# Performance work log

Measured on AMD Instinct MI355X. Metric: run time of the kernel, lower is better.

## Reference

```python
import jax, jax.numpy as jnp
import numpy as np

B, K, D = 131072, 1024, 128  # batch, codebook size, code dim


def setup_inputs() -> dict:
    key = jax.random.key(0)
    k1, k2 = jax.random.split(key)
    z_e = jax.random.normal(k1, (B, D), dtype=jnp.float32)
    # nn.Embedding weight init: uniform(-1/K, 1/K) as in TactileVQ.__init__
    codebook = jax.random.uniform(k2, (K, D), dtype=jnp.float32,
                                  minval=-1.0 / K, maxval=1.0 / K)
    return {"z_e": z_e, "codebook": codebook}


def reference(z_e, codebook):
    """TactileVQ forward: cdist(p=2) -> argmin -> codebook gather -> commitment MSE.
    Squared distances share the same argmin as euclidean cdist, so we use the
    expansion ||z||^2 - 2 z.E^T + ||E||^2 and never take a sqrt.
    """
    z_sq = jnp.sum(z_e * z_e, axis=-1, keepdims=True)          # [B, 1]
    e_sq = jnp.sum(codebook * codebook, axis=-1)               # [K]
    # [B, K] squared distances (monotone transform of cdist p=2)
    d2 = z_sq - 2.0 * jnp.einsum('bd,kd->bk', z_e, codebook) + e_sq
    encoding_indices = jnp.argmin(d2, axis=-1)                 # [B] int
    z_q = codebook[encoding_indices]                           # [B, D] gather
    commitment_loss = jnp.mean(
        (z_q - jax.lax.stop_gradient(z_e)) ** 2)               # mse vs detached z_e
    return z_q, commitment_loss, encoding_indices
```

## Files before the change

### kernel.cpp

```cpp
#include <hip/hip_runtime.h>
#include <math.h>

#define BN 131072
#define KN 1024
#define DN 128
#define GCODES 64
#define NGRP (KN / GCODES)

#define FROWS 256
#define FBLK (BN / FROWS)

#define ROWS 64
#define NBLK (BN / ROWS)

#define TAMB 2.5e-4f
#define CANARY 0.01f

typedef __attribute__((ext_vector_type(8))) short s16x8;
typedef __attribute__((ext_vector_type(4))) short s16x4;
typedef __attribute__((ext_vector_type(4))) float f32x4;

__device__ __forceinline__ unsigned short f2bf(float f) {
    const unsigned int u = __float_as_uint(f);
    return (unsigned short)((u + 0x7fffu + ((u >> 16) & 1u)) >> 16);
}
__device__ __forceinline__ float bf2f(unsigned short s) {
    return __uint_as_float(((unsigned int)s) << 16);
}
__device__ __forceinline__ void cvt4(const float4 v, s16x4& h4, s16x4& l4) {
    const unsigned short h0 = f2bf(v.x), h1 = f2bf(v.y), h2 = f2bf(v.z), h3 = f2bf(v.w);
    h4[0] = (short)h0; h4[1] = (short)h1; h4[2] = (short)h2; h4[3] = (short)h3;
    l4[0] = (short)f2bf(v.x - bf2f(h0));
    l4[1] = (short)f2bf(v.y - bf2f(h1));
    l4[2] = (short)f2bf(v.z - bf2f(h2));
    l4[3] = (short)f2bf(v.w - bf2f(h3));
}
__device__ __forceinline__ void cvt8(const float4 v0, const float4 v1,
                                     s16x8& h, s16x8& l) {
    s16x4 h0, l0, h1, l1;
    cvt4(v0, h0, l0); cvt4(v1, h1, l1);
    h[0]=h0[0]; h[1]=h0[1]; h[2]=h0[2]; h[3]=h0[3];
    h[4]=h1[0]; h[5]=h1[1]; h[6]=h1[2]; h[7]=h1[3];
    l[0]=l0[0]; l[1]=l0[1]; l[2]=l0[2]; l[3]=l0[3];
// ... 60 lines not shown
            a8[1] = __fadd_rn(a8[1], __fmul_rn(v0.y, v0.y));
            a8[2] = __fadd_rn(a8[2], __fmul_rn(v0.z, v0.z));
            a8[3] = __fadd_rn(a8[3], __fmul_rn(v0.w, v0.w));
            a8[4] = __fadd_rn(a8[4], __fmul_rn(v1.x, v1.x));
            a8[5] = __fadd_rn(a8[5], __fmul_rn(v1.y, v1.y));
            a8[6] = __fadd_rn(a8[6], __fmul_rn(v1.z, v1.z));
            a8[7] = __fadd_rn(a8[7], __fmul_rn(v1.w, v1.w));
        }
    }
    zsq[row] = __fadd_rn(
        __fadd_rn(__fadd_rn(a8[0], a8[1]), __fadd_rn(a8[2], a8[3])),
        __fadd_rn(__fadd_rn(a8[4], a8[5]), __fadd_rn(a8[6], a8[7])));
}

__device__ __forceinline__ float exact_d2_g(const float* __restrict__ z,
                                            const float* __restrict__ cb,
                                            const int grow, const int k,
                                            const float zsq, const float ek) {
    const float* zr = z + (size_t)grow * DN;
    const float* cr = cb + (size_t)k * DN;
    float dot = 0.0f;
#pragma unroll
    for (int j = 0; j < 32; ++j) {
        const float4 zv = *reinterpret_cast<const float4*>(zr + j * 4);
        const float4 cv = *reinterpret_cast<const float4*>(cr + j * 4);
        dot = __fmaf_rn(zv.x, cv.x, dot);
        dot = __fmaf_rn(zv.y, cv.y, dot);
        dot = __fmaf_rn(zv.z, cv.z, dot);
        dot = __fmaf_rn(zv.w, cv.w, dot);
    }
    return __fadd_rn(__fsub_rn(zsq, __fmul_rn(2.0f, dot)), ek);
}

__device__ __forceinline__ void tile_compute(const s16x8 (&ch)[4][4],
                                             const s16x8 (&cl)[4][4],
                                             const s16x8 (&zh)[4],
                                             const s16x8 (&zl)[4],
                                             const float (&ekv)[16],
                                             const int kbase, const int r0,
                                             float4* __restrict__ pq,
                                             const int l15, const int l4h) {
    f32x4 acc[4];
#pragma unroll
    for (int ct = 0; ct < 4; ++ct) acc[ct] = (f32x4){0.0f, 0.0f, 0.0f, 0.0f};
#pragma unroll
    for (int ks = 0; ks < 4; ++ks) {
#pragma unroll
        for (int ct = 0; ct < 4; ++ct) {
            acc[ct] = __builtin_amdgcn_mfma_f32_16x16x32_bf16(ch[ct][ks], zh[ks], acc[ct], 0, 0, 0);
            acc[ct] = __builtin_amdgcn_mfma_f32_16x16x32_bf16(cl[ct][ks], zh[ks], acc[ct], 0, 0, 0);
            acc[ct] = __builtin_amdgcn_mfma_f32_16x16x32_bf16(ch[ct][ks], zl[ks], acc[ct], 0, 0, 0);
        }
    }
    float b1 = INFINITY, b2 = INFINITY, b3 = INFINITY;
    int   i1 = 0, i2 = 0;
#pragma unroll
    for (int ct = 0; ct < 4; ++ct) {
#pragma unroll
        for (int e = 0; e < 4; ++e) {
            const float sc = __fmaf_rn(-2.0f, acc[ct][e], ekv[ct * 4 + e]);
            const int   kk = kbase + ct * 16 + l4h * 4 + e;
            const bool lt1 = sc < b1;
            const bool lt2 = sc < b2;
            const bool lt3 = sc < b3;
            b3 = lt2 ? b2 : (lt3 ? sc : b3);
            b2 = lt1 ? b1 : (lt2 ? sc : b2);
            i2 = lt1 ? i1 : (lt2 ? kk : i2);
            b1 = lt1 ? sc : b1;
            i1 = lt1 ? kk : i1;
        }
    }
#pragma unroll
    for (int st = 16; st < 64; st <<= 1) {
        const float ob1 = __shfl_xor(b1, st);
        const int   oi1 = __shfl_xor(i1, st);
        const float ob2 = __shfl_xor(b2, st);
        const int   oi2 = __shfl_xor(i2, st);
        const float ob3 = __shfl_xor(b3, st);
        float v1, v2, v3; int j1, j2;
        if (ob1 < b1) {
            v1 = ob1; j1 = oi1;
            if (b1 < ob2) { v2 = b1;  j2 = i1;  v3 = fminf(b2, ob2); }
            else          { v2 = ob2; j2 = oi2; v3 = fminf(b1, ob3); }
        } else {
            v1 = b1; j1 = i1;
            if (ob1 < b2) { v2 = ob1; j2 = oi1; v3 = fminf(ob2, b2); }
            else          { v2 = b2;  j2 = i2;  v3 = fminf(ob1, b3); }
        }
        b1 = v1; i1 = j1; b2 = v2; i2 = j2; b3 = v3;
    }
    if (l4h == 0) {
        float4 q;
        q.x = b1; q.y = b2; q.z = b3;
        q.w = __int_as_float((i2 << 16) | i1);
        pq[r0 + l15] = q;
    }
}

__device__ __forceinline__ void tile_load_zp(const unsigned short* __restrict__ zb,
                                             s16x8 (&zh)[4], s16x8 (&zl)[4]) {
#pragma unroll
    for (int ks = 0; ks < 4; ++ks) {
        zh[ks] = *reinterpret_cast<const s16x8*>(zb + ks * 512);
        zl[ks] = *reinterpret_cast<const s16x8*>(zb + 2048 + ks * 512);
    }
}

__global__ __launch_bounds__(256, 2) void vq_score_pre(const unsigned short* __restrict__ zp,
                                                       const unsigned short* __restrict__ planes,
                                                       const float* __restrict__ esq,
                                                       float4* __restrict__ pquad) {
    const int tid  = threadIdx.x;
    const int lane = tid & 63;
    const int w    = tid >> 6;
    const int l15  = lane & 15;
    const int l4h  = lane >> 4;
    const int sliceW = blockIdx.x >> 7;
    const int chunk  = blockIdx.x & 127;
    const int sub    = sliceW * 4 + w;
    const int kbase  = sub * 64;

    s16x8 ch[4][4], cl[4][4];
    {
        const unsigned short* gp = planes + (size_t)sub * 16384;
#pragma unroll
        for (int ks = 0; ks < 4; ++ks)
#pragma unroll
            for (int ct = 0; ct < 4; ++ct) {
                const int off = ((((ks * 4 + l4h) << 6) + (ct << 4) + l15) << 3);
                ch[ct][ks] = *reinterpret_cast<const s16x8*>(gp + off);
                cl[ct][ks] = *reinterpret_cast<const s16x8*>(gp + 8192 + off);
            }
    }
    float ekv[16];
#pragma unroll
    for (int ct = 0; ct < 4; ++ct)
#pragma unroll
        for (int e = 0; e < 4; ++e)
            ekv[ct * 4 + e] = esq[kbase + ct * 16 + l4h * 4 + e];

    const int cbase = chunk * 64;
    const int rbase = chunk * 1024;
    float4* pq = pquad + (size_t)sub * BN;
    const unsigned short* zpl = zp + l4h * 128 + l15 * 8;

    s16x8 hA[4], lA[4], hB[4], lB[4];
    tile_load_zp(zpl + (size_t)cbase * 4096, hA, lA);
#pragma unroll 1
    for (int t = 0; t < 64; t += 2) {
        tile_load_zp(zpl + (size_t)(cbase + t + 1) * 4096, hB, lB);
        tile_compute(ch, cl, hA, lA, ekv, kbase, rbase + t * 16, pq, l15, l4h);
        const int tn = (t + 2 < 64) ? t + 2 : 63;
        tile_load_zp(zpl + (size_t)(cbase + tn) * 4096, hA, lA);
        tile_compute(ch, cl, hB, lB, ekv, kbase, rbase + (t + 1) * 16, pq, l15, l4h);
    }
}

__global__ __launch_bounds__(256, 2) void vq_score(const float* __restrict__ z,
                                                   const unsigned short* __restrict__ planes,
                                                   const float* __restrict__ esq,
                                                   float4* __restrict__ pquad) {
    const int tid  = threadIdx.x;
    const int lane = tid & 63;
    const int w    = tid >> 6;
    const int l15  = lane & 15;
    const int l4h  = lane >> 4;
    const int sliceW = blockIdx.x >> 7;
    const int chunk  = blockIdx.x & 127;
    const int sub    = sliceW * 4 + w;
    const int kbase  = sub * 64;

    s16x8 ch[4][4], cl[4][4];
    {
        const unsigned short* gp = planes + (size_t)sub * 16384;
#pragma unroll
        for (int ks = 0; ks < 4; ++ks)
#pragma unroll
            for (int ct = 0; ct < 4; ++ct) {
                const int off = ((((ks * 4 + l4h) << 6) + (ct << 4) + l15) << 3);
                ch[ct][ks] = *reinterpret_cast<const s16x8*>(gp + off);
                cl[ct][ks] = *reinterpret_cast<const s16x8*>(gp + 8192 + off);
            }
    }
    float ekv[16];
#pragma unroll
    for (int ct = 0; ct < 4; ++ct)
#pragma unroll
        for (int e = 0; e < 4; ++e)
            ekv[ct * 4 + e] = esq[kbase + ct * 16 + l4h * 4 + e];

    const int rbase = chunk * 1024;
    float4* pq = pquad + (size_t)sub * BN;

#pragma unroll 1
    for (int t = 0; t < 64; ++t) {
        const int r0 = rbase + t * 16;
        s16x8 zh[4], zl[4];
#pragma unroll
        for (int ks = 0; ks < 4; ++ks) {
            const float* src = z + (size_t)(r0 + l15) * DN + ks * 32 + l4h * 8;
            const float4 v0 = *reinterpret_cast<const float4*>(src);
            const float4 v1 = *reinterpret_cast<const float4*>(src + 4);
            cvt8(v0, v1, zh[ks], zl[ks]);
        }
        tile_compute(ch, cl, zh, zl, ekv, kbase, r0, pq, l15, l4h);
    }
}

template <bool HZ>
__global__ __launch_bounds__(256, 2) void vq_finish2(const float* __restrict__ z,
                                                     const float* __restrict__ cb,
                                                     const float* __restrict__ esq,
                                                     const float* __restrict__ zsqArr,
                                                     const float4* __restrict__ pquad,
                                                     float* __restrict__ out,
                                                     double* __restrict__ partials) {
    __shared__ __align__(16) float sEsq[KN];
    __shared__ float  szsq[FROWS];
    __shared__ int    sbidx[FROWS], sI1[FROWS], sI2[FROWS];
    __shared__ int    t2list[FROWS], t3list[FROWS];
    __shared__ int    t2n, t3n, sbad;
    __shared__ double sls[256];

    const int tid  = threadIdx.x;
    const int lane = tid & 63;
    const int w    = tid >> 6;
    const int row0 = blockIdx.x * FROWS;

    if (tid == 0) { t2n = 0; t3n = 0; sbad = 0; }
#pragma unroll
    for (int i = 0; i < 4; ++i) sEsq[i * 256 + tid] = esq[i * 256 + tid];

    if constexpr (HZ) {
        szsq[tid] = zsqArr[row0 + tid];
    } else {
        const float* zr = z + (size_t)(row0 + tid) * DN;
        float a8[8];
#pragma unroll
        for (int c = 0; c < 32; ++c) {
            const float4 v = *reinterpret_cast<const float4*>(zr + c * 4);
            const int t0 = 4 * (c & 1);
            if (c < 2) {
                a8[t0 + 0] = __fmul_rn(v.x, v.x);
                a8[t0 + 1] = __fmul_rn(v.y, v.y);
                a8[t0 + 2] = __fmul_rn(v.z, v.z);
                a8[t0 + 3] = __fmul_rn(v.w, v.w);
            } else {
                a8[t0 + 0] = __fadd_rn(a8[t0 + 0], __fmul_rn(v.x, v.x));
                a8[t0 + 1] = __fadd_rn(a8[t0 + 1], __fmul_rn(v.y, v.y));
                a8[t0 + 2] = __fadd_rn(a8[t0 + 2], __fmul_rn(v.z, v.z));
                a8[t0 + 3] = __fadd_rn(a8[t0 + 3], __fmul_rn(v.w, v.w));
            }
        }
        szsq[tid] = __fadd_rn(
            __fadd_rn(__fadd_rn(a8[0], a8[1]), __fadd_rn(a8[2], a8[3])),
            __fadd_rn(__fadd_rn(a8[4], a8[5]), __fadd_rn(a8[6], a8[7])));
    }
    __syncthreads();

    float B1 = INFINITY, B2 = INFINITY, B3 = INFINITY;
    int   I1 = 0, I2 = 0;
    {
        const int r = row0 + tid;
#pragma unroll
        for (int s = 0; s < 16; ++s) {
            const float4 q = pquad[(size_t)s * BN + r];
            const int ii = __float_as_int(q.w);
            const int j1 = ii & 0xffff, j2 = ii >> 16;
            if (q.x < B1)      { B3 = B2; B2 = B1; I2 = I1; B1 = q.x; I1 = j1; }
            else if (q.x < B2) { B3 = B2; B2 = q.x; I2 = j1; }
            else if (q.x < B3) { B3 = q.x; }
            if (q.y < B2)      { B3 = B2; B2 = q.y; I2 = j2; }
            else if (q.y < B3) { B3 = q.y; }
            B3 = fminf(B3, q.z);
        }
        sbidx[tid] = I1; sI1[tid] = I1; sI2[tid] = I2;
        if ((tid & 63) == 0) {
            const float d2x  = exact_d2_g(z, cb, r, I1, szsq[tid], sEsq[I1]);
            const float pred = __fadd_rn(szsq[tid], B1);
            if (fabsf(pred - d2x) > CANARY) sbad = 1;
        }
    }
    __syncthreads();

    if (sbad) {
        for (int r = w; r < FROWS; r += 4) {
            const float zsq = szsq[r];
            float best = INFINITY; int bi = 0;
#pragma unroll 1
            for (int kk = 0; kk < 16; ++kk) {
                const int k = lane * 16 + kk;
                const float d2v = exact_d2_g(z, cb, row0 + r, k, zsq, sEsq[k]);
                if (d2v < best) { best = d2v; bi = k; }
            }
#pragma unroll
            for (int m = 1; m < 64; m <<= 1) {
                const float ob  = __shfl_xor(best, m);
                const int   obi = __shfl_xor(bi, m);
                if (ob < best || (ob == best && obi < bi)) { best = ob; bi = obi; }
            }
            if (lane == 0) sbidx[r] = bi;
        }
    } else {
        if (B3 - B1 <= TAMB) {
            const int p = atomicAdd(&t3n, 1); t3list[p] = tid;
        } else if (B2 - B1 <= TAMB) {
            const int p = atomicAdd(&t2n, 1); t2list[p] = tid;
        }
    }
    __syncthreads();

    if (tid < t2n) {
        const int r  = t2list[tid];
        const int ka = sI1[r], kb = sI2[r];
        const float zsq = szsq[r];
        const float da = exact_d2_g(z, cb, row0 + r, ka, zsq, sEsq[ka]);
        const float db = exact_d2_g(z, cb, row0 + r, kb, zsq, sEsq[kb]);
        int win;
        if (da < db) win = ka;
        else if (db < da) win = kb;
        else win = (ka < kb) ? ka : kb;
        sbidx[r] = win;
    }
    for (int ii = w; ii < t3n; ii += 4) {
        const int r = t3list[ii];
        const float zsq = szsq[r];
        float best = INFINITY; int bi = 0;
#pragma unroll 1
        for (int kk = 0; kk < 16; ++kk) {
            const int k = lane * 16 + kk;
            const float d2v = exact_d2_g(z, cb, row0 + r, k, zsq, sEsq[k]);
            if (d2v < best) { best = d2v; bi = k; }
        }
#pragma unroll
        for (int m = 1; m < 64; m <<= 1) {
            const float ob  = __shfl_xor(best, m);
            const int   obi = __shfl_xor(bi, m);
            if (ob < best || (ob == best && obi < bi)) { best = ob; bi = obi; }
        }
        if (lane == 0) sbidx[r] = bi;
    }
    __syncthreads();

    out[(size_t)BN * DN + 1 + row0 + tid] = (float)sbidx[tid];

    double ls = 0.0;
#pragma unroll
    for (int it = 0; it < 32; ++it) {
        const int r = it * 8 + (tid >> 5);
        const int j = tid & 31;
        const float4 zv = *reinterpret_cast<const float4*>(
            z + ((size_t)(row0 + r)) * DN + j * 4);
        const int bfin = sbidx[r];
        const float4 cv = *reinterpret_cast<const float4*>(
            cb + ((size_t)bfin) * DN + j * 4);
        *reinterpret_cast<float4*>(out + ((size_t)(row0 + r)) * DN + j * 4) = cv;
        const float d0 = __fsub_rn(cv.x, zv.x);
        const float d1 = __fsub_rn(cv.y, zv.y);
        const float d2e = __fsub_rn(cv.z, zv.z);
        const float d3 = __fsub_rn(cv.w, zv.w);
        ls += (double)__fmul_rn(d0, d0);
        ls += (double)__fmul_rn(d1, d1);
        ls += (double)__fmul_rn(d2e, d2e);
        ls += (double)__fmul_rn(d3, d3);
    }
    sls[tid] = ls;
    __syncthreads();
    for (int s = 128; s > 0; s >>= 1) {
        if (tid < s) sls[tid] += sls[tid + s];
        __syncthreads();
    }
    if (tid == 0) partials[blockIdx.x] = sls[0];
}

#define UPD(s, sc, kk) { \
    const bool lt1 = (sc) < b1v[s]; \
    const bool lt2 = (sc) < b2v[s]; \
    const bool lt3 = (sc) < b3v[s]; \
    b3v[s] = lt2 ? b2v[s] : (lt3 ? (sc) : b3v[s]); \
    b2v[s] = lt1 ? b1v[s] : (lt2 ? (sc) : b2v[s]); \
    i2v[s] = lt1 ? i1v[s] : (lt2 ? (kk) : i2v[s]); \
    b1v[s] = lt1 ? (sc) : b1v[s]; \
    i1v[s] = lt1 ? (kk) : i1v[s]; }

__global__ __launch_bounds__(256, 2) void vq_lds(const float* __restrict__ z,
                                                 const float* __restrict__ cb,
                                                 const float* __restrict__ esq,
                                                 float* __restrict__ out,
                                                 double* __restrict__ partials) {
    __shared__ __align__(16) short cbS[2][16384];
    __shared__ __align__(16) float sEsq[KN];
    __shared__ float  szsq[ROWS];
    __shared__ float  sB1[2][ROWS], sB2[2][ROWS], sB3[2][ROWS];
    __shared__ int    sI1[2][ROWS], sI2[2][ROWS];
    __shared__ int    sbidx[ROWS];
    __shared__ int    t2list[ROWS], t3list[ROWS];
    __shared__ int    t2n, t3n;
// ... 285 lines not shown
__global__ __launch_bounds__(256) void loss_kernel(const double* __restrict__ partials,
                                                   float* __restrict__ out, int n) {
    __shared__ double s[256];
    double acc = 0.0;
    for (int i = threadIdx.x; i < n; i += 256) acc += partials[i];
    s[threadIdx.x] = acc;
    __syncthreads();
    for (int t = 128; t > 0; t >>= 1) {
        if (threadIdx.x < t) s[threadIdx.x] += s[threadIdx.x + t];
        __syncthreads();
    }
    if (threadIdx.x == 0)
        out[(size_t)BN * DN] = (float)(s[0] / ((double)BN * (double)DN));
}

extern "C" void kernel_launch(void* const* d_in, const int* in_sizes, int n_in,
                              void* d_out, int out_size, void* d_ws, size_t ws_size,
                              hipStream_t stream) {
    const float* z  = (const float*)d_in[0];
    const float* cb = (const float*)d_in[1];
    float* out = (float*)d_out;

    float*          esq      = (float*)d_ws;
    double*         partials = (double*)((char*)d_ws + 4096);
    unsigned short* cbpl     = (unsigned short*)((char*)d_ws + 20480);
    float4*         pquad    = (float4*)((char*)d_ws + 544768);
    float*          zsqArr   = (float*)((char*)d_ws + 34099200ull);
    unsigned short* zpl      = (unsigned short*)((char*)d_ws + 34623488ull);
    const size_t need_mid  = 34099200ull;
    const size_t need_full = 101732352ull;

    esq_kernel<<<KN / 256, 256, 0, stream>>>(cb, esq);
    if (ws_size >= need_full) {
        cvt_kernel <<<64, 256, 0, stream>>>(cb, cbpl);
        zprep_kernel<<<BN / 256, 256, 0, stream>>>(z, zpl, zsqArr);
        vq_score_pre<<<512, 256, 0, stream>>>(zpl, cbpl, esq, pquad);
        vq_finish2<true><<<FBLK, 256, 0, stream>>>(z, cb, esq, zsqArr, pquad, out, partials);
        loss_kernel<<<1, 256, 0, stream>>>(partials, out, FBLK);
    } else if (ws_size >= need_mid) {
        cvt_kernel<<<64, 256, 0, stream>>>(cb, cbpl);
        vq_score  <<<512, 256, 0, stream>>>(z, cbpl, esq, pquad);
        vq_finish2<false><<<FBLK, 256, 0, stream>>>(z, cb, esq, nullptr, pquad, out, partials);
        loss_kernel<<<1, 256, 0, stream>>>(partials, out, FBLK);
    } else {
        vq_lds<<<NBLK, 256, 0, stream>>>(z, cb, esq, out, partials);
        loss_kernel<<<1, 256, 0, stream>>>(partials, out, NBLK);
    }
}
```

Baseline: 261.0 us.

## Split finish-kernel candidate merge across two thread halves and raise MFMA priority

The finish kernel now handles 128 rows per block instead of 256. Each row's 16 partial top-3 candidate lists are split between two threads, each scanning 8 of them, and the halves are merged through shared memory. This doubles the number of blocks and raises the occupancy hint so more loads are in flight. It also moves tie classification before the first barrier, removing one sync, and wraps the MFMA block in s_setprio so matrix instructions get issue priority. The cost is the extra LDS traffic for the merge, with half the threads idle during scalar phases.

```diff
diff --git a/kernel.cpp b/kernel.cpp
--- a/kernel.cpp
+++ b/kernel.cpp
@@ -7,8 +7,8 @@
 #define GCODES 64
 #define NGRP (KN / GCODES)
 
-#define FROWS 256
-#define FBLK (BN / FROWS)
+#define F3ROWS 128
+#define F3BLK (BN / F3ROWS)
 
 #define ROWS 64
 #define NBLK (BN / ROWS)
@@ -146,6 +146,7 @@
     f32x4 acc[4];
 #pragma unroll
     for (int ct = 0; ct < 4; ++ct) acc[ct] = (f32x4){0.0f, 0.0f, 0.0f, 0.0f};
+    __builtin_amdgcn_s_setprio(1);
 #pragma unroll
     for (int ks = 0; ks < 4; ++ks) {
 #pragma unroll
@@ -155,6 +156,7 @@
             acc[ct] = __builtin_amdgcn_mfma_f32_16x16x32_bf16(ch[ct][ks], zl[ks], acc[ct], 0, 0, 0);
         }
     }
+    __builtin_amdgcn_s_setprio(0);
     float b1 = INFINITY, b2 = INFINITY, b3 = INFINITY;
     int   i1 = 0, i2 = 0;
 #pragma unroll
@@ -311,7 +313,7 @@
 }
 
 template <bool HZ>
-__global__ __launch_bounds__(256, 2) void vq_finish2(const float* __restrict__ z,
+__global__ __launch_bounds__(256, 4) void vq_finish3(const float* __restrict__ z,
                                                      const float* __restrict__ cb,
                                                      const float* __restrict__ esq,
                                                      const float* __restrict__ zsqArr,
@@ -319,75 +321,106 @@
                                                      float* __restrict__ out,
                                                      double* __restrict__ partials) {
     __shared__ __align__(16) float sEsq[KN];
-    __shared__ float  szsq[FROWS];
-    __shared__ int    sbidx[FROWS], sI1[FROWS], sI2[FROWS];
-    __shared__ int    t2list[FROWS], t3list[FROWS];
+    __shared__ float  szsq[F3ROWS];
+    __shared__ float  hB1[F3ROWS], hB2[F3ROWS], hB3[F3ROWS];
+    __shared__ int    hI1[F3ROWS], hI2[F3ROWS];
+    __shared__ int    sbidx[F3ROWS], sI1[F3ROWS], sI2[F3ROWS];
+    __shared__ int    t2list[F3ROWS], t3list[F3ROWS];
     __shared__ int    t2n, t3n, sbad;
     __shared__ double sls[256];
 
-    const int tid  = threadIdx.x;
-    const int lane = tid & 63;
-    const int w    = tid >> 6;
-    const int row0 = blockIdx.x * FROWS;
+    const int tid   = threadIdx.x;
+    const int lane  = tid & 63;
+    const int w     = tid >> 6;
+    const int rloc  = tid & 127;
+    const int shalf = tid >> 7;
+    const int row0  = blockIdx.x * F3ROWS;
 
     if (tid == 0) { t2n = 0; t3n = 0; sbad = 0; }
 #pragma unroll
     for (int i = 0; i < 4; ++i) sEsq[i * 256 + tid] = esq[i * 256 + tid];
 
-    if constexpr (HZ) {
-        szsq[tid] = zsqArr[row0 + tid];
-    } else {
-        const float* zr = z + (size_t)(row0 + tid) * DN;
-        float a8[8];
-#pragma unroll
-        for (int c = 0; c < 32; ++c) {
-            const float4 v = *reinterpret_cast<const float4*>(zr + c * 4);
-            const int t0 = 4 * (c & 1);
-            if (c < 2) {
-                a8[t0 + 0] = __fmul_rn(v.x, v.x);
-                a8[t0 + 1] = __fmul_rn(v.y, v.y);
-                a8[t0 + 2] = __fmul_rn(v.z, v.z);
-                a8[t0 + 3] = __fmul_rn(v.w, v.w);
-            } else {
-                a8[t0 + 0] = __fadd_rn(a8[t0 + 0], __fmul_rn(v.x, v.x));
-                a8[t0 + 1] = __fadd_rn(a8[t0 + 1], __fmul_rn(v.y, v.y));
-                a8[t0 + 2] = __fadd_rn(a8[t0 + 2], __fmul_rn(v.z, v.z));
-                a8[t0 + 3] = __fadd_rn(a8[t0 + 3], __fmul_rn(v.w, v.w));
-            }
-        }
-        szsq[tid] = __fadd_rn(
-            __fadd_rn(__fadd_rn(a8[0], a8[1]), __fadd_rn(a8[2], a8[3])),
-            __fadd_rn(__fadd_rn(a8[4], a8[5]), __fadd_rn(a8[6], a8[7])));
-    }
-    __syncthreads();
-
-    float B1 = INFINITY, B2 = INFINITY, B3 = INFINITY;
-    int   I1 = 0, I2 = 0;
+    if (tid < F3ROWS) {
+        if constexpr (HZ) {
+            szsq[tid] = zsqArr[row0 + tid];
+        } else {
+            const float* zr = z + (size_t)(row0 + tid) * DN;
+            float a8[8];
+#pragma unroll
+            for (int c = 0; c < 32; ++c) {
+                const float4 v = *reinterpret_cast<const float4*>(zr + c * 4);
+                const int t0 = 4 * (c & 1);
+                if (c < 2) {
+                    a8[t0 + 0] = __fmul_rn(v.x, v.x);
+                    a8[t0 + 1] = __fmul_rn(v.y, v.y);
+                    a8[t0 + 2] = __fmul_rn(v.z, v.z);
+                    a8[t0 + 3] = __fmul_rn(v.w, v.w);
+                } else {
+                    a8[t0 + 0] = __fadd_rn(a8[t0 + 0], __fmul_rn(v.x, v.x));
+                    a8[t0 + 1] = __fadd_rn(a8[t0 + 1], __fmul_rn(v.y, v.y));
+                    a8[t0 + 2] = __fadd_rn(a8[t0 + 2], __fmul_rn(v.z, v.z));
+                    a8[t0 + 3] = __fadd_rn(a8[t0 + 3], __fmul_rn(v.w, v.w));
+                }
+            }
+            szsq[tid] = __fadd_rn(
+                __fadd_rn(__fadd_rn(a8[0], a8[1]), __fadd_rn(a8[2], a8[3])),
+                __fadd_rn(__fadd_rn(a8[4], a8[5]), __fadd_rn(a8[6], a8[7])));
+        }
+    }
+
+    float b1 = INFINITY, b2 = INFINITY, b3 = INFINITY;
+    int   i1 = 0, i2 = 0;
     {
-        const int r = row0 + tid;
-#pragma unroll
-        for (int s = 0; s < 16; ++s) {
-            const float4 q = pquad[(size_t)s * BN + r];
+        const int r  = row0 + rloc;
+        const int s0 = shalf * 8;
+#pragma unroll
+        for (int s = 0; s < 8; ++s) {
+            const float4 q = pquad[(size_t)(s0 + s) * BN + r];
             const int ii = __float_as_int(q.w);
             const int j1 = ii & 0xffff, j2 = ii >> 16;
-            if (q.x < B1)      { B3 = B2; B2 = B1; I2 = I1; B1 = q.x; I1 = j1; }
-            else if (q.x < B2) { B3 = B2; B2 = q.x; I2 = j1; }
-            else if (q.x < B3) { B3 = q.x; }
-            if (q.y < B2)      { B3 = B2; B2 = q.y; I2 = j2; }
-            else if (q.y < B3) { B3 = q.y; }
-            B3 = fminf(B3, q.z);
+            if (q.x < b1)      { b3 = b2; b2 = b1; i2 = i1; b1 = q.x; i1 = j1; }
+            else if (q.x < b2) { b3 = b2; b2 = q.x; i2 = j1; }
+            else if (q.x < b3) { b3 = q.x; }
+            if (q.y < b2)      { b3 = b2; b2 = q.y; i2 = j2; }
+            else if (q.y < b3) { b3 = q.y; }
+            b3 = fminf(b3, q.z);
+        }
+    }
+    if (shalf) {
+        hB1[rloc] = b1; hB2[rloc] = b2; hB3[rloc] = b3;
+        hI1[rloc] = i1; hI2[rloc] = i2;
+    }
+    __syncthreads();
+
+    float B1, B2, B3; int I1, I2;
+    if (tid < F3ROWS) {
+        const float c1 = hB1[tid], c2 = hB2[tid], c3 = hB3[tid];
+        const int  cj1 = hI1[tid], cj2 = hI2[tid];
+        if (b1 <= c1) {
+            B1 = b1; I1 = i1;
+            if (b2 <= c1) { B2 = b2; I2 = i2;  B3 = fminf(b3, c1); }
+            else          { B2 = c1; I2 = cj1; B3 = fminf(b2, c2); }
+        } else {
+            B1 = c1; I1 = cj1;
+            if (c2 <= b1) { B2 = c2; I2 = cj2; B3 = fminf(c3, b1); }
+            else          { B2 = b1; I2 = i1;  B3 = fminf(c2, b2); }
         }
         sbidx[tid] = I1; sI1[tid] = I1; sI2[tid] = I2;
         if ((tid & 63) == 0) {
-            const float d2x  = exact_d2_g(z, cb, r, I1, szsq[tid], sEsq[I1]);
+            const float d2x  = exact_d2_g(z, cb, row0 + tid, I1, szsq[tid], sEsq[I1]);
             const float pred = __fadd_rn(szsq[tid], B1);
             if (fabsf(pred - d2x) > CANARY) sbad = 1;
         }
+        if (B3 - B1 <= TAMB) {
+            const int p = atomicAdd(&t3n, 1); t3list[p] = tid;
+        } else if (B2 - B1 <= TAMB) {
+            const int p = atomicAdd(&t2n, 1); t2list[p] = tid;
+        }
     }
     __syncthreads();
 
     if (sbad) {
-        for (int r = w; r < FROWS; r += 4) {
+        for (int r = w; r < F3ROWS; r += 4) {
             const float zsq = szsq[r];
             float best = INFINITY; int bi = 0;
 #pragma unroll 1
@@ -405,51 +438,45 @@
             if (lane == 0) sbidx[r] = bi;
         }
     } else {
-        if (B3 - B1 <= TAMB) {
-            const int p = atomicAdd(&t3n, 1); t3list[p] = tid;
-        } else if (B2 - B1 <= TAMB) {
-            const int p = atomicAdd(&t2n, 1); t2list[p] = tid;
-        }
-    }
-    __syncthreads();
-
-    if (tid < t2n) {
-        const int r  = t2list[tid];
-        const int ka = sI1[r], kb = sI2[r];
-        const float zsq = szsq[r];
-        const float da = exact_d2_g(z, cb, row0 + r, ka, zsq, sEsq[ka]);
-        const float db = exact_d2_g(z, cb, row0 + r, kb, zsq, sEsq[kb]);
-        int win;
-        if (da < db) win = ka;
-        else if (db < da) win = kb;
-        else win = (ka < kb) ? ka : kb;
-        sbidx[r] = win;
-    }
-    for (int ii = w; ii < t3n; ii += 4) {
-        const int r = t3list[ii];
-        const float zsq = szsq[r];
-        float best = INFINITY; int bi = 0;
+        if (tid < t2n) {
+            const int r  = t2list[tid];
+            const int ka = sI1[r], kb = sI2[r];
+            const float zsq = szsq[r];
+            const float da = exact_d2_g(z, cb, row0 + r, ka, zsq, sEsq[ka]);
+            const float db = exact_d2_g(z, cb, row0 + r, kb, zsq, sEsq[kb]);
+            int win;
+            if (da < db) win = ka;
+            else if (db < da) win = kb;
+            else win = (ka < kb) ? ka : kb;
+            sbidx[r] = win;
+        }
+        for (int ii = w; ii < t3n; ii += 4) {
+            const int r = t3list[ii];
+            const float zsq = szsq[r];
+            float best = INFINITY; int bi = 0;
 #pragma unroll 1
-        for (int kk = 0; kk < 16; ++kk) {
-            const int k = lane * 16 + kk;
-            const float d2v = exact_d2_g(z, cb, row0 + r, k, zsq, sEsq[k]);
-            if (d2v < best) { best = d2v; bi = k; }
-        }
-#pragma unroll
-        for (int m = 1; m < 64; m <<= 1) {
-            const float ob  = __shfl_xor(best, m);
-            const int   obi = __shfl_xor(bi, m);
-            if (ob < best || (ob == best && obi < bi)) { best = ob; bi = obi; }
-        }
-        if (lane == 0) sbidx[r] = bi;
-    }
-    __syncthreads();
-
-    out[(size_t)BN * DN + 1 + row0 + tid] = (float)sbidx[tid];
+            for (int kk = 0; kk < 16; ++kk) {
+                const int k = lane * 16 + kk;
+                const float d2v = exact_d2_g(z, cb, row0 + r, k, zsq, sEsq[k]);
+                if (d2v < best) { best = d2v; bi = k; }
+            }
+#pragma unroll
+            for (int m = 1; m < 64; m <<= 1) {
+                const float ob  = __shfl_xor(best, m);
+                const int   obi = __shfl_xor(bi, m);
+                if (ob < best || (ob == best && obi < bi)) { best = ob; bi = obi; }
+            }
+            if (lane == 0) sbidx[r] = bi;
+        }
+    }
+    __syncthreads();
+
+    if (tid < F3ROWS)
+        out[(size_t)BN * DN + 1 + row0 + tid] = (float)sbidx[tid];
 
     double ls = 0.0;
 #pragma unroll
-    for (int it = 0; it < 32; ++it) {
+    for (int it = 0; it < 16; ++it) {
         const int r = it * 8 + (tid >> 5);
         const int j = tid & 31;
         const float4 zv = *reinterpret_cast<const float4*>(
@@ -820,13 +847,13 @@
         cvt_kernel <<<64, 256, 0, stream>>>(cb, cbpl);
         zprep_kernel<<<BN / 256, 256, 0, stream>>>(z, zpl, zsqArr);
         vq_score_pre<<<512, 256, 0, stream>>>(zpl, cbpl, esq, pquad);
-        vq_finish2<true><<<FBLK, 256, 0, stream>>>(z, cb, esq, zsqArr, pquad, out, partials);
-        loss_kernel<<<1, 256, 0, stream>>>(partials, out, FBLK);
+        vq_finish3<true><<<F3BLK, 256, 0, stream>>>(z, cb, esq, zsqArr, pquad, out, partials);
+        loss_kernel<<<1, 256, 0, stream>>>(partials, out, F3BLK);
     } else if (ws_size >= need_mid) {
         cvt_kernel<<<64, 256, 0, stream>>>(cb, cbpl);
         vq_score  <<<512, 256, 0, stream>>>(z, cbpl, esq, pquad);
-        vq_finish2<false><<<FBLK, 256, 0, stream>>>(z, cb, esq, nullptr, pquad, out, partials);
-        loss_kernel<<<1, 256, 0, stream>>>(partials, out, FBLK);
+        vq_finish3<false><<<F3BLK, 256, 0, stream>>>(z, cb, esq, nullptr, pquad, out, partials);
+        loss_kernel<<<1, 256, 0, stream>>>(partials, out, F3BLK);
     } else {
         vq_lds<<<NBLK, 256, 0, stream>>>(z, cb, esq, out, partials);
         loss_kernel<<<1, 256, 0, stream>>>(partials, out, NBLK);
```

After: 279.2 us. 7.0% more time.

## Stage codebook slice in LDS, split finish into merge and epilogue kernels

Applied to the files above, without the earlier changes.

The scoring kernel now loads each 64-code bf16 hi/lo slice into shared memory instead of registers. It raises occupancy to 3 blocks per SM, processes two z tiles per iteration sharing the codebook fragment loads, and wraps the MFMA loop in s_setprio. The finish kernel is split into a merge kernel that writes indices and a separate epilogue that gathers codes, writes z_q and reduces the loss over smaller 64-row blocks. The merge also prefetches all 16 partial quads before reducing them. This trades register pressure for LDS reads and adds a launch plus a round trip of the indices through global memory.

```diff
diff --git a/kernel.cpp b/kernel.cpp
--- a/kernel.cpp
+++ b/kernel.cpp
@@ -7,8 +7,11 @@
 #define GCODES 64
 #define NGRP (KN / GCODES)
 
-#define FROWS 256
-#define FBLK (BN / FROWS)
+#define MROWS 256
+#define MBLK (BN / MROWS)
+
+#define EROWS 64
+#define EBLK (BN / EROWS)
 
 #define ROWS 64
 #define NBLK (BN / ROWS)
@@ -135,26 +138,11 @@
     return __fadd_rn(__fsub_rn(zsq, __fmul_rn(2.0f, dot)), ek);
 }
 
-__device__ __forceinline__ void tile_compute(const s16x8 (&ch)[4][4],
-                                             const s16x8 (&cl)[4][4],
-                                             const s16x8 (&zh)[4],
-                                             const s16x8 (&zl)[4],
-                                             const float (&ekv)[16],
-                                             const int kbase, const int r0,
-                                             float4* __restrict__ pq,
-                                             const int l15, const int l4h) {
-    f32x4 acc[4];
-#pragma unroll
-    for (int ct = 0; ct < 4; ++ct) acc[ct] = (f32x4){0.0f, 0.0f, 0.0f, 0.0f};
-#pragma unroll
-    for (int ks = 0; ks < 4; ++ks) {
-#pragma unroll
-        for (int ct = 0; ct < 4; ++ct) {
-            acc[ct] = __builtin_amdgcn_mfma_f32_16x16x32_bf16(ch[ct][ks], zh[ks], acc[ct], 0, 0, 0);
-            acc[ct] = __builtin_amdgcn_mfma_f32_16x16x32_bf16(cl[ct][ks], zh[ks], acc[ct], 0, 0, 0);
-            acc[ct] = __builtin_amdgcn_mfma_f32_16x16x32_bf16(ch[ct][ks], zl[ks], acc[ct], 0, 0, 0);
-        }
-    }
+__device__ __forceinline__ void fin_store(const f32x4 (&acc)[4],
+                                          const float (&ekv)[16],
+                                          const int kbase, const int r0,
+                                          float4* __restrict__ pq,
+                                          const int l15, const int l4h) {
     float b1 = INFINITY, b2 = INFINITY, b3 = INFINITY;
     int   i1 = 0, i2 = 0;
 #pragma unroll
@@ -200,62 +188,78 @@
     }
 }
 
-__device__ __forceinline__ void tile_load_zp(const unsigned short* __restrict__ zb,
-                                             s16x8 (&zh)[4], s16x8 (&zl)[4]) {
-#pragma unroll
-    for (int ks = 0; ks < 4; ++ks) {
-        zh[ks] = *reinterpret_cast<const s16x8*>(zb + ks * 512);
-        zl[ks] = *reinterpret_cast<const s16x8*>(zb + 2048 + ks * 512);
-    }
-}
-
-__global__ __launch_bounds__(256, 2) void vq_score_pre(const unsigned short* __restrict__ zp,
-                                                       const unsigned short* __restrict__ planes,
+__global__ __launch_bounds__(256, 3) void vq_score_lds(const unsigned short* __restrict__ zp,
+                                                       const unsigned short* __restrict__ cbpl,
                                                        const float* __restrict__ esq,
                                                        float4* __restrict__ pquad) {
+    __shared__ __align__(16) short cbS[16384];
     const int tid  = threadIdx.x;
     const int lane = tid & 63;
     const int w    = tid >> 6;
     const int l15  = lane & 15;
     const int l4h  = lane >> 4;
-    const int sliceW = blockIdx.x >> 7;
-    const int chunk  = blockIdx.x & 127;
-    const int sub    = sliceW * 4 + w;
-    const int kbase  = sub * 64;
-
-    s16x8 ch[4][4], cl[4][4];
+    const int sub   = blockIdx.x >> 7;
+    const int chunk = blockIdx.x & 127;
+    const int kbase = sub * 64;
+
     {
-        const unsigned short* gp = planes + (size_t)sub * 16384;
-#pragma unroll
-        for (int ks = 0; ks < 4; ++ks)
+        const float4* src = reinterpret_cast<const float4*>(cbpl + (size_t)sub * 16384);
+        float4* dst = reinterpret_cast<float4*>(cbS);
+#pragma unroll
+        for (int i = 0; i < 8; ++i)
+            dst[i * 256 + tid] = src[i * 256 + tid];
+    }
+    float ekv[16];
+#pragma unroll
+    for (int ct = 0; ct < 4; ++ct)
+#pragma unroll
+        for (int e = 0; e < 4; ++e)
+            ekv[ct * 4 + e] = esq[kbase + ct * 16 + l4h * 4 + e];
+    __syncthreads();
+
+    const int tbase = chunk * 64 + w * 16;
+    float4* pq = pquad + (size_t)sub * BN;
+    const unsigned short* zpl = zp + l4h * 128 + l15 * 8;
+
+#pragma unroll 1
+    for (int tp = 0; tp < 16; tp += 2) {
+        s16x8 zh[2][4], zl[2][4];
+#pragma unroll
+        for (int u = 0; u < 2; ++u) {
+            const unsigned short* zb = zpl + (size_t)(tbase + tp + u) * 4096;
+#pragma unroll
+            for (int ks = 0; ks < 4; ++ks) {
+                zh[u][ks] = *reinterpret_cast<const s16x8*>(zb + ks * 512);
+                zl[u][ks] = *reinterpret_cast<const s16x8*>(zb + 2048 + ks * 512);
+            }
+        }
+        f32x4 acc[2][4];
+#pragma unroll
+        for (int u = 0; u < 2; ++u)
+#pragma unroll
+            for (int ct = 0; ct < 4; ++ct)
+                acc[u][ct] = (f32x4){0.0f, 0.0f, 0.0f, 0.0f};
+
+        __builtin_amdgcn_s_setprio(1);
+#pragma unroll
+        for (int ks = 0; ks < 4; ++ks) {
 #pragma unroll
             for (int ct = 0; ct < 4; ++ct) {
                 const int off = ((((ks * 4 + l4h) << 6) + (ct << 4) + l15) << 3);
-                ch[ct][ks] = *reinterpret_cast<const s16x8*>(gp + off);
-                cl[ct][ks] = *reinterpret_cast<const s16x8*>(gp + 8192 + off);
-            }
-    }
-    float ekv[16];
-#pragma unroll
-    for (int ct = 0; ct < 4; ++ct)
-#pragma unroll
-        for (int e = 0; e < 4; ++e)
-            ekv[ct * 4 + e] = esq[kbase + ct * 16 + l4h * 4 + e];
-
-    const int cbase = chunk * 64;
-    const int rbase = chunk * 1024;
-    float4* pq = pquad + (size_t)sub * BN;
-    const unsigned short* zpl = zp + l4h * 128 + l15 * 8;
-
-    s16x8 hA[4], lA[4], hB[4], lB[4];
-    tile_load_zp(zpl + (size_t)cbase * 4096, hA, lA);
-#pragma unroll 1
-    for (int t = 0; t < 64; t += 2) {
-        tile_load_zp(zpl + (size_t)(cbase + t + 1) * 4096, hB, lB);
-        tile_compute(ch, cl, hA, lA, ekv, kbase, rbase + t * 16, pq, l15, l4h);
-        const int tn = (t + 2 < 64) ? t + 2 : 63;
-        tile_load_zp(zpl + (size_t)(cbase + tn) * 4096, hA, lA);
-        tile_compute(ch, cl, hB, lB, ekv, kbase, rbase + (t + 1) * 16, pq, l15, l4h);
+                const s16x8 bh = *reinterpret_cast<const s16x8*>(&cbS[off]);
+                const s16x8 bl = *reinterpret_cast<const s16x8*>(&cbS[8192 + off]);
+                acc[0][ct] = __builtin_amdgcn_mfma_f32_16x16x32_bf16(bh, zh[0][ks], acc[0][ct], 0, 0, 0);
+                acc[0][ct] = __builtin_amdgcn_mfma_f32_16x16x32_bf16(bl, zh[0][ks], acc[0][ct], 0, 0, 0);
+                acc[0][ct] = __builtin_amdgcn_mfma_f32_16x16x32_bf16(bh, zl[0][ks], acc[0][ct], 0, 0, 0);
+                acc[1][ct] = __builtin_amdgcn_mfma_f32_16x16x32_bf16(bh, zh[1][ks], acc[1][ct], 0, 0, 0);
+                acc[1][ct] = __builtin_amdgcn_mfma_f32_16x16x32_bf16(bl, zh[1][ks], acc[1][ct], 0, 0, 0);
+                acc[1][ct] = __builtin_amdgcn_mfma_f32_16x16x32_bf16(bh, zl[1][ks], acc[1][ct], 0, 0, 0);
+            }
+        }
+        __builtin_amdgcn_s_setprio(0);
+
+        fin_store(acc[0], ekv, kbase, (tbase + tp) * 16,     pq, l15, l4h);
+        fin_store(acc[1], ekv, kbase, (tbase + tp + 1) * 16, pq, l15, l4h);
     }
 }
 
@@ -306,29 +310,41 @@
             const float4 v1 = *reinterpret_cast<const float4*>(src + 4);
             cvt8(v0, v1, zh[ks], zl[ks]);
         }
-        tile_compute(ch, cl, zh, zl, ekv, kbase, r0, pq, l15, l4h);
+        f32x4 acc[4];
+#pragma unroll
+        for (int ct = 0; ct < 4; ++ct) acc[ct] = (f32x4){0.0f, 0.0f, 0.0f, 0.0f};
+        __builtin_amdgcn_s_setprio(1);
+#pragma unroll
+        for (int ks = 0; ks < 4; ++ks) {
+#pragma unroll
+            for (int ct = 0; ct < 4; ++ct) {
+                acc[ct] = __builtin_amdgcn_mfma_f32_16x16x32_bf16(ch[ct][ks], zh[ks], acc[ct], 0, 0, 0);
+                acc[ct] = __builtin_amdgcn_mfma_f32_16x16x32_bf16(cl[ct][ks], zh[ks], acc[ct], 0, 0, 0);
+                acc[ct] = __builtin_amdgcn_mfma_f32_16x16x32_bf16(ch[ct][ks], zl[ks], acc[ct], 0, 0, 0);
+            }
+        }
+        __builtin_amdgcn_s_setprio(0);
+        fin_store(acc, ekv, kbase, r0, pq, l15, l4h);
     }
 }
 
 template <bool HZ>
-__global__ __launch_bounds__(256, 2) void vq_finish2(const float* __restrict__ z,
-                                                     const float* __restrict__ cb,
-                                                     const float* __restrict__ esq,
-                                                     const float* __restrict__ zsqArr,
-                                                     const float4* __restrict__ pquad,
-                                                     float* __restrict__ out,
-                                                     double* __restrict__ partials) {
+__global__ __launch_bounds__(256, 2) void vq_merge(const float* __restrict__ z,
+                                                   const float* __restrict__ cb,
+                                                   const float* __restrict__ esq,
+                                                   const float* __restrict__ zsqArr,
+                                                   const float4* __restrict__ pquad,
+                                                   float* __restrict__ out) {
     __shared__ __align__(16) float sEsq[KN];
-    __shared__ float  szsq[FROWS];
-    __shared__ int    sbidx[FROWS], sI1[FROWS], sI2[FROWS];
-    __shared__ int    t2list[FROWS], t3list[FROWS];
+    __shared__ float  szsq[MROWS];
+    __shared__ int    sbidx[MROWS], sI1[MROWS], sI2[MROWS];
+    __shared__ int    t2list[MROWS], t3list[MROWS];
     __shared__ int    t2n, t3n, sbad;
-    __shared__ double sls[256];
 
     const int tid  = threadIdx.x;
     const int lane = tid & 63;
     const int w    = tid >> 6;
-    const int row0 = blockIdx.x * FROWS;
+    const int row0 = blockIdx.x * MROWS;
 
     if (tid == 0) { t2n = 0; t3n = 0; sbad = 0; }
 #pragma unroll
@@ -365,17 +381,20 @@
     int   I1 = 0, I2 = 0;
     {
         const int r = row0 + tid;
+        float4 q[16];
+#pragma unroll
+        for (int s = 0; s < 16; ++s)
+            q[s] = pquad[(size_t)s * BN + r];
 #pragma unroll
         for (int s = 0; s < 16; ++s) {
-            const float4 q = pquad[(size_t)s * BN + r];
-            const int ii = __float_as_int(q.w);
+            const int ii = __float_as_int(q[s].w);
             const int j1 = ii & 0xffff, j2 = ii >> 16;
-            if (q.x < B1)      { B3 = B2; B2 = B1; I2 = I1; B1 = q.x; I1 = j1; }
-            else if (q.x < B2) { B3 = B2; B2 = q.x; I2 = j1; }
-            else if (q.x < B3) { B3 = q.x; }
-            if (q.y < B2)      { B3 = B2; B2 = q.y; I2 = j2; }
-            else if (q.y < B3) { B3 = q.y; }
-            B3 = fminf(B3, q.z);
+            if (q[s].x < B1)      { B3 = B2; B2 = B1; I2 = I1; B1 = q[s].x; I1 = j1; }
+            else if (q[s].x < B2) { B3 = B2; B2 = q[s].x; I2 = j1; }
+            else if (q[s].x < B3) { B3 = q[s].x; }
+            if (q[s].y < B2)      { B3 = B2; B2 = q[s].y; I2 = j2; }
+            else if (q[s].y < B3) { B3 = q[s].y; }
+            B3 = fminf(B3, q[s].z);
         }
         sbidx[tid] = I1; sI1[tid] = I1; sI2[tid] = I2;
         if ((tid & 63) == 0) {
@@ -387,7 +406,7 @@
     __syncthreads();
 
     if (sbad) {
-        for (int r = w; r < FROWS; r += 4) {
+        for (int r = w; r < MROWS; r += 4) {
             const float zsq = szsq[r];
             float best = INFINITY; int bi = 0;
 #pragma unroll 1
@@ -446,26 +465,48 @@
     __syncthreads();
 
     out[(size_t)BN * DN + 1 + row0 + tid] = (float)sbidx[tid];
+}
+
+__global__ __launch_bounds__(256, 4) void vq_epilogue(const float* __restrict__ z,
+                                                      const float* __restrict__ cb,
+                                                      float* __restrict__ out,
+                                                      double* __restrict__ partials) {
+    __shared__ int sidx[EROWS];
+    __shared__ double sls[256];
+    const int tid  = threadIdx.x;
+    const int row0 = blockIdx.x * EROWS;
+
+    if (tid < EROWS)
+        sidx[tid] = (int)out[(size_t)BN * DN + 1 + row0 + tid];
+    __syncthreads();
 
     double ls = 0.0;
-#pragma unroll
-    for (int it = 0; it < 32; ++it) {
-        const int r = it * 8 + (tid >> 5);
-        const int j = tid & 31;
-        const float4 zv = *reinterpret_cast<const float4*>(
-            z + ((size_t)(row0 + r)) * DN + j * 4);
-        const int bfin = sbidx[r];
-        const float4 cv = *reinterpret_cast<const float4*>(
-            cb + ((size_t)bfin) * DN + j * 4);
-        *reinterpret_cast<float4*>(out + ((size_t)(row0 + r)) * DN + j * 4) = cv;
-        const float d0 = __fsub_rn(cv.x, zv.x);
-        const float d1 = __fsub_rn(cv.y, zv.y);
-        const float d2e = __fsub_rn(cv.z, zv.z);
-        const float d3 = __fsub_rn(cv.w, zv.w);
-        ls += (double)__fmul_rn(d0, d0);
-        ls += (double)__fmul_rn(d1, d1);
-        ls += (double)__fmul_rn(d2e, d2e);
-        ls += (double)__fmul_rn(d3, d3);
+    const int j = tid & 31;
+#pragma unroll
+    for (int half = 0; half < 2; ++half) {
+        float4 zb[4], cv[4];
+        int rr[4];
+#pragma unroll
+        for (int u = 0; u < 4; ++u) {
+            const int it = half * 4 + u;
+            rr[u] = it * 8 + (tid >> 5);
+            zb[u] = *reinterpret_cast<const float4*>(
+                z + (size_t)(row0 + rr[u]) * DN + j * 4);
+            cv[u] = *reinterpret_cast<const float4*>(
+                cb + (size_t)sidx[rr[u]] * DN + j * 4);
+        }
+#pragma unroll
+        for (int u = 0; u < 4; ++u) {
+            *reinterpret_cast<float4*>(out + (size_t)(row0 + rr[u]) * DN + j * 4) = cv[u];
+            const float d0 = __fsub_rn(cv[u].x, zb[u].x);
+            const float d1 = __fsub_rn(cv[u].y, zb[u].y);
+            const float d2e = __fsub_rn(cv[u].z, zb[u].z);
+            const float d3 = __fsub_rn(cv[u].w, zb[u].w);
+            ls += (double)__fmul_rn(d0, d0);
+            ls += (double)__fmul_rn(d1, d1);
+            ls += (double)__fmul_rn(d2e, d2e);
+            ls += (double)__fmul_rn(d3, d3);
+        }
     }
     sls[tid] = ls;
     __syncthreads();
@@ -817,16 +858,18 @@
 
     esq_kernel<<<KN / 256, 256, 0, stream>>>(cb, esq);
     if (ws_size >= need_full) {
-        cvt_kernel <<<64, 256, 0, stream>>>(cb, cbpl);
+        cvt_kernel  <<<64, 256, 0, stream>>>(cb, cbpl);
         zprep_kernel<<<BN / 256, 256, 0, stream>>>(z, zpl, zsqArr);
-        vq_score_pre<<<512, 256, 0, stream>>>(zpl, cbpl, esq, pquad);
-        vq_finish2<true><<<FBLK, 256, 0, stream>>>(z, cb, esq, zsqArr, pquad, out, partials);
-        loss_kernel<<<1, 256, 0, stream>>>(partials, out, FBLK);
+        vq_score_lds<<<2048, 256, 0, stream>>>(zpl, cbpl, esq, pquad);
+        vq_merge<true><<<MBLK, 256, 0, stream>>>(z, cb, esq, zsqArr, pquad, out);
+        vq_epilogue <<<EBLK, 256, 0, stream>>>(z, cb, out, partials);
+        loss_kernel <<<1, 256, 0, stream>>>(partials, out, EBLK);
     } else if (ws_size >= need_mid) {
         cvt_kernel<<<64, 256, 0, stream>>>(cb, cbpl);
         vq_score  <<<512, 256, 0, stream>>>(z, cbpl, esq, pquad);
-        vq_finish2<false><<<FBLK, 256, 0, stream>>>(z, cb, esq, nullptr, pquad, out, partials);
-        loss_kernel<<<1, 256, 0, stream>>>(partials, out, FBLK);
+        vq_merge<false><<<MBLK, 256, 0, stream>>>(z, cb, esq, nullptr, pquad, out);
+        vq_epilogue<<<EBLK, 256, 0, stream>>>(z, cb, out, partials);
+        loss_kernel<<<1, 256, 0, stream>>>(partials, out, EBLK);
     } else {
         vq_lds<<<NBLK, 256, 0, stream>>>(z, cb, esq, out, partials);
         loss_kernel<<<1, 256, 0, stream>>>(partials, out, NBLK);
```

After: 555.5 us. +112.8%, slower.

## Split finish kernel into merge and epilogue kernels with smaller blocks

Applied to the files above, without the earlier changes.

Splits the combined finish kernel into two launches. vq_merge uses 128-row blocks to merge the partial top-k scores and refine ambiguous rows; it reads esq straight from global memory instead of staging it in LDS, and batches its pquad loads. vq_epilogue uses 64-row blocks to do the codebook gather, the output write and the loss partials, reading the indices back from the output buffer. The aim is more blocks and better latency hiding in the memory-bound tail, at the cost of an extra launch and re-reading the indices.

```diff
diff --git a/kernel.cpp b/kernel.cpp
--- a/kernel.cpp
+++ b/kernel.cpp
@@ -7,8 +7,11 @@
 #define GCODES 64
 #define NGRP (KN / GCODES)
 
-#define FROWS 256
-#define FBLK (BN / FROWS)
+#define MROWS 128
+#define MBLK (BN / MROWS)
+
+#define EROWS 64
+#define EBLK (BN / EROWS)
 
 #define ROWS 64
 #define NBLK (BN / ROWS)
@@ -311,33 +314,29 @@
 }
 
 template <bool HZ>
-__global__ __launch_bounds__(256, 2) void vq_finish2(const float* __restrict__ z,
-                                                     const float* __restrict__ cb,
-                                                     const float* __restrict__ esq,
-                                                     const float* __restrict__ zsqArr,
-                                                     const float4* __restrict__ pquad,
-                                                     float* __restrict__ out,
-                                                     double* __restrict__ partials) {
-    __shared__ __align__(16) float sEsq[KN];
-    __shared__ float  szsq[FROWS];
-    __shared__ int    sbidx[FROWS], sI1[FROWS], sI2[FROWS];
-    __shared__ int    t2list[FROWS], t3list[FROWS];
+__global__ __launch_bounds__(128, 4) void vq_merge(const float* __restrict__ z,
+                                                   const float* __restrict__ cb,
+                                                   const float* __restrict__ esq,
+                                                   const float* __restrict__ zsqArr,
+                                                   const float4* __restrict__ pquad,
+                                                   float* __restrict__ out) {
+    __shared__ float  szsq[MROWS];
+    __shared__ int    sbidx[MROWS], sI1[MROWS], sI2[MROWS];
+    __shared__ int    t2list[MROWS], t3list[MROWS];
     __shared__ int    t2n, t3n, sbad;
-    __shared__ double sls[256];
 
     const int tid  = threadIdx.x;
     const int lane = tid & 63;
     const int w    = tid >> 6;
-    const int row0 = blockIdx.x * FROWS;
+    const int row0 = blockIdx.x * MROWS;
+    const int r    = row0 + tid;
 
     if (tid == 0) { t2n = 0; t3n = 0; sbad = 0; }
-#pragma unroll
-    for (int i = 0; i < 4; ++i) sEsq[i * 256 + tid] = esq[i * 256 + tid];
 
     if constexpr (HZ) {
-        szsq[tid] = zsqArr[row0 + tid];
+        szsq[tid] = zsqArr[r];
     } else {
-        const float* zr = z + (size_t)(row0 + tid) * DN;
+        const float* zr = z + (size_t)r * DN;
         float a8[8];
 #pragma unroll
         for (int c = 0; c < 32; ++c) {
@@ -363,37 +362,40 @@
 
     float B1 = INFINITY, B2 = INFINITY, B3 = INFINITY;
     int   I1 = 0, I2 = 0;
-    {
-        const int r = row0 + tid;
-#pragma unroll
-        for (int s = 0; s < 16; ++s) {
-            const float4 q = pquad[(size_t)s * BN + r];
-            const int ii = __float_as_int(q.w);
+#pragma unroll
+    for (int half = 0; half < 2; ++half) {
+        float4 q[8];
+#pragma unroll
+        for (int s = 0; s < 8; ++s)
+            q[s] = pquad[(size_t)(half * 8 + s) * BN + r];
+#pragma unroll
+        for (int s = 0; s < 8; ++s) {
+            const int ii = __float_as_int(q[s].w);
             const int j1 = ii & 0xffff, j2 = ii >> 16;
-            if (q.x < B1)      { B3 = B2; B2 = B1; I2 = I1; B1 = q.x; I1 = j1; }
-            else if (q.x < B2) { B3 = B2; B2 = q.x; I2 = j1; }
-            else if (q.x < B3) { B3 = q.x; }
-            if (q.y < B2)      { B3 = B2; B2 = q.y; I2 = j2; }
-            else if (q.y < B3) { B3 = q.y; }
-            B3 = fminf(B3, q.z);
-        }
-        sbidx[tid] = I1; sI1[tid] = I1; sI2[tid] = I2;
-        if ((tid & 63) == 0) {
-            const float d2x  = exact_d2_g(z, cb, r, I1, szsq[tid], sEsq[I1]);
-            const float pred = __fadd_rn(szsq[tid], B1);
-            if (fabsf(pred - d2x) > CANARY) sbad = 1;
-        }
+            if (q[s].x < B1)      { B3 = B2; B2 = B1; I2 = I1; B1 = q[s].x; I1 = j1; }
+            else if (q[s].x < B2) { B3 = B2; B2 = q[s].x; I2 = j1; }
+            else if (q[s].x < B3) { B3 = q[s].x; }
+            if (q[s].y < B2)      { B3 = B2; B2 = q[s].y; I2 = j2; }
+            else if (q[s].y < B3) { B3 = q[s].y; }
+            B3 = fminf(B3, q[s].z);
+        }
+    }
+    sbidx[tid] = I1; sI1[tid] = I1; sI2[tid] = I2;
+    if ((tid & 63) == 0) {
+        const float d2x  = exact_d2_g(z, cb, r, I1, szsq[tid], esq[I1]);
+        const float pred = __fadd_rn(szsq[tid], B1);
+        if (fabsf(pred - d2x) > CANARY) sbad = 1;
     }
     __syncthreads();
 
     if (sbad) {
-        for (int r = w; r < FROWS; r += 4) {
-            const float zsq = szsq[r];
+        for (int rr = w; rr < MROWS; rr += 2) {
+            const float zsq = szsq[rr];
             float best = INFINITY; int bi = 0;
 #pragma unroll 1
             for (int kk = 0; kk < 16; ++kk) {
                 const int k = lane * 16 + kk;
-                const float d2v = exact_d2_g(z, cb, row0 + r, k, zsq, sEsq[k]);
+                const float d2v = exact_d2_g(z, cb, row0 + rr, k, zsq, esq[k]);
                 if (d2v < best) { best = d2v; bi = k; }
             }
 #pragma unroll
@@ -402,7 +404,7 @@
                 const int   obi = __shfl_xor(bi, m);
                 if (ob < best || (ob == best && obi < bi)) { best = ob; bi = obi; }
             }
-            if (lane == 0) sbidx[r] = bi;
+            if (lane == 0) sbidx[rr] = bi;
         }
     } else {
         if (B3 - B1 <= TAMB) {
@@ -414,25 +416,25 @@
     __syncthreads();
 
     if (tid < t2n) {
-        const int r  = t2list[tid];
-        const int ka = sI1[r], kb = sI2[r];
-        const float zsq = szsq[r];
-        const float da = exact_d2_g(z, cb, row0 + r, ka, zsq, sEsq[ka]);
-        const float db = exact_d2_g(z, cb, row0 + r, kb, zsq, sEsq[kb]);
+        const int rr = t2list[tid];
+        const int ka = sI1[rr], kb = sI2[rr];
+        const float zsq = szsq[rr];
+        const float da = exact_d2_g(z, cb, row0 + rr, ka, zsq, esq[ka]);
+        const float db = exact_d2_g(z, cb, row0 + rr, kb, zsq, esq[kb]);
         int win;
         if (da < db) win = ka;
         else if (db < da) win = kb;
         else win = (ka < kb) ? ka : kb;
-        sbidx[r] = win;
-    }
-    for (int ii = w; ii < t3n; ii += 4) {
-        const int r = t3list[ii];
-        const float zsq = szsq[r];
+        sbidx[rr] = win;
+    }
+    for (int ii = w; ii < t3n; ii += 2) {
+        const int rr = t3list[ii];
+        const float zsq = szsq[rr];
         float best = INFINITY; int bi = 0;
 #pragma unroll 1
         for (int kk = 0; kk < 16; ++kk) {
             const int k = lane * 16 + kk;
-            const float d2v = exact_d2_g(z, cb, row0 + r, k, zsq, sEsq[k]);
+            const float d2v = exact_d2_g(z, cb, row0 + rr, k, zsq, esq[k]);
             if (d2v < best) { best = d2v; bi = k; }
         }
 #pragma unroll
@@ -441,31 +443,53 @@
             const int   obi = __shfl_xor(bi, m);
             if (ob < best || (ob == best && obi < bi)) { best = ob; bi = obi; }
         }
-        if (lane == 0) sbidx[r] = bi;
-    }
-    __syncthreads();
-
-    out[(size_t)BN * DN + 1 + row0 + tid] = (float)sbidx[tid];
+        if (lane == 0) sbidx[rr] = bi;
+    }
+    __syncthreads();
+
+    out[(size_t)BN * DN + 1 + r] = (float)sbidx[tid];
+}
+
+__global__ __launch_bounds__(256, 4) void vq_epilogue(const float* __restrict__ z,
+                                                      const float* __restrict__ cb,
+                                                      float* __restrict__ out,
+                                                      double* __restrict__ partials) {
+    __shared__ int sidx[EROWS];
+    __shared__ double sls[256];
+    const int tid  = threadIdx.x;
+    const int row0 = blockIdx.x * EROWS;
+
+    if (tid < EROWS)
+        sidx[tid] = (int)out[(size_t)BN * DN + 1 + row0 + tid];
+    __syncthreads();
 
     double ls = 0.0;
-#pragma unroll
-    for (int it = 0; it < 32; ++it) {
-        const int r = it * 8 + (tid >> 5);
-        const int j = tid & 31;
-        const float4 zv = *reinterpret_cast<const float4*>(
-            z + ((size_t)(row0 + r)) * DN + j * 4);
-        const int bfin = sbidx[r];
-        const float4 cv = *reinterpret_cast<const float4*>(
-            cb + ((size_t)bfin) * DN + j * 4);
-        *reinterpret_cast<float4*>(out + ((size_t)(row0 + r)) * DN + j * 4) = cv;
-        const float d0 = __fsub_rn(cv.x, zv.x);
-        const float d1 = __fsub_rn(cv.y, zv.y);
-        const float d2e = __fsub_rn(cv.z, zv.z);
-        const float d3 = __fsub_rn(cv.w, zv.w);
-        ls += (double)__fmul_rn(d0, d0);
-        ls += (double)__fmul_rn(d1, d1);
-        ls += (double)__fmul_rn(d2e, d2e);
-        ls += (double)__fmul_rn(d3, d3);
+    const int j = tid & 31;
+#pragma unroll
+    for (int half = 0; half < 2; ++half) {
+        float4 zb[4], cv[4];
+        int rr[4];
+#pragma unroll
+        for (int u = 0; u < 4; ++u) {
+            const int it = half * 4 + u;
+            rr[u] = it * 8 + (tid >> 5);
+            zb[u] = *reinterpret_cast<const float4*>(
+                z + (size_t)(row0 + rr[u]) * DN + j * 4);
+            cv[u] = *reinterpret_cast<const float4*>(
+                cb + (size_t)sidx[rr[u]] * DN + j * 4);
+        }
+#pragma unroll
+        for (int u = 0; u < 4; ++u) {
+            *reinterpret_cast<float4*>(out + (size_t)(row0 + rr[u]) * DN + j * 4) = cv[u];
+            const float d0 = __fsub_rn(cv[u].x, zb[u].x);
+            const float d1 = __fsub_rn(cv[u].y, zb[u].y);
+            const float d2e = __fsub_rn(cv[u].z, zb[u].z);
+            const float d3 = __fsub_rn(cv[u].w, zb[u].w);
+            ls += (double)__fmul_rn(d0, d0);
+            ls += (double)__fmul_rn(d1, d1);
+            ls += (double)__fmul_rn(d2e, d2e);
+            ls += (double)__fmul_rn(d3, d3);
+        }
     }
     sls[tid] = ls;
     __syncthreads();
@@ -817,16 +841,18 @@
 
     esq_kernel<<<KN / 256, 256, 0, stream>>>(cb, esq);
     if (ws_size >= need_full) {
-        cvt_kernel <<<64, 256, 0, stream>>>(cb, cbpl);
+        cvt_kernel  <<<64, 256, 0, stream>>>(cb, cbpl);
         zprep_kernel<<<BN / 256, 256, 0, stream>>>(z, zpl, zsqArr);
         vq_score_pre<<<512, 256, 0, stream>>>(zpl, cbpl, esq, pquad);
-        vq_finish2<true><<<FBLK, 256, 0, stream>>>(z, cb, esq, zsqArr, pquad, out, partials);
-        loss_kernel<<<1, 256, 0, stream>>>(partials, out, FBLK);
+        vq_merge<true><<<MBLK, 128, 0, stream>>>(z, cb, esq, zsqArr, pquad, out);
+        vq_epilogue <<<EBLK, 256, 0, stream>>>(z, cb, out, partials);
+        loss_kernel <<<1, 256, 0, stream>>>(partials, out, EBLK);
     } else if (ws_size >= need_mid) {
         cvt_kernel<<<64, 256, 0, stream>>>(cb, cbpl);
         vq_score  <<<512, 256, 0, stream>>>(z, cbpl, esq, pquad);
-        vq_finish2<false><<<FBLK, 256, 0, stream>>>(z, cb, esq, nullptr, pquad, out, partials);
-        loss_kernel<<<1, 256, 0, stream>>>(partials, out, FBLK);
+        vq_merge<false><<<MBLK, 128, 0, stream>>>(z, cb, esq, nullptr, pquad, out);
+        vq_epilogue<<<EBLK, 256, 0, stream>>>(z, cb, out, partials);
+        loss_kernel<<<1, 256, 0, stream>>>(partials, out, EBLK);
     } else {
         vq_lds<<<NBLK, 256, 0, stream>>>(z, cb, esq, out, partials);
         loss_kernel<<<1, 256, 0, stream>>>(partials, out, NBLK);
```

Result: slower. 322.6 us (+23.6%).
